# Kernel tuning notes

Measured on AMD Instinct MI355X. Metric: run time of the kernel, lower is better.

## Reference

```python
import jax, jax.numpy as jnp
from jax import lax
import numpy as np

B, TQ, T = 64, 2, 2048
HID, ENC, U, FILT, K = 1024, 512, 256, 32, 31


def setup_inputs() -> dict:
    key = jax.random.key(0)
    ks = jax.random.split(key, 12)
    def w(k, shape, fan_in):
        return jax.random.normal(k, shape, jnp.float32) / np.sqrt(fan_in)
    return {
        "query": jax.random.normal(ks[0], (B, TQ, HID), jnp.float32),
        "state": jax.random.uniform(ks[1], (B, T), jnp.float32),
        "memory": jax.random.normal(ks[2], (B, T, ENC), jnp.float32),
        "Wq": w(ks[3], (HID, U), HID), "bq": jnp.zeros((U,), jnp.float32),
        "Wm": w(ks[4], (ENC, U), ENC), "bm": jnp.zeros((U,), jnp.float32),
        "Wl": w(ks[5], (FILT, U), FILT), "bl": jnp.zeros((U,), jnp.float32),
        "conv_w": w(ks[6], (FILT, 1, K), K), "conv_b": jnp.zeros((FILT,), jnp.float32),
        "We": w(ks[7], (U, U), U), "be": jnp.zeros((U,), jnp.float32),
        "v_a": w(ks[8], (U,), U),
    }


def reference(query, state, memory, Wq, bq, Wm, bm, Wl, bl, conv_w, conv_b, We, be, v_a):
    # memory projection (done in `initialize` in the original): [B,T,U]
    mem_proj = jnp.einsum("bte,eu->btu", memory, Wm) + bm
    # query projection then slice timestep 1 -> [B,1,U]
    pq = (jnp.einsum("bqh,hu->bqu", query, Wq) + bq)[:, 1:2, :]
    # location features: 1-D conv over time of previous alignment, 'same' padding
    x = state[:, None, :]                                    # [B,1,T]
    f = lax.conv_general_dilated(x, conv_w, (1,), "SAME",
                                 dimension_numbers=("NCH", "OIH", "NCH"))
    f = f + conv_b[None, :, None]                            # [B,FILT,T]
    loc = jnp.einsum("bft,fu->btu", f, Wl) + bl              # [B,T,U]
    # additive energy with tanh, reduced against v_a -> [B,T]
    h = jnp.tanh(jnp.einsum("btu,uv->btv", pq + loc + mem_proj, We) + be)
    energy = jnp.einsum("btu,u->bt", h, v_a)
    # smoothing normalization: sigmoid / sum(sigmoid)
    s = jax.nn.sigmoid(energy)
    alignment = s / jnp.sum(s, axis=-1, keepdims=True)
    # cumulate_weights=True: accumulate onto previous alignment
    cum_alignment = state + alignment
    # context against projected memory: [B,1,U]
    context = jnp.einsum("bt,btu->bu", cum_alignment, mem_proj)[:, None, :]
    return context
```

## Files before the change

kernel.cpp:

```cpp
#include <hip/hip_runtime.h>
#include <math.h>

#define Bq 64
#define Tt 2048
#define TQn 2
#define HIDn 1024
#define ENCn 512
#define Un 256
#define FILTn 32
#define KKn 31

#define TTILE 32
#define NCHUNK (Tt / TTILE)
#define LDK 520

typedef short short8 __attribute__((ext_vector_type(8)));
typedef float f32x4  __attribute__((ext_vector_type(4)));
typedef unsigned short ushort_t;
typedef unsigned int   uint_t;

__device__ __forceinline__ ushort_t f2b(float f) {
    union { float f; uint_t u; } x; x.f = f;
    uint_t r = x.u + 0x7fffu + ((x.u >> 16) & 1u);
    return (ushort_t)(r >> 16);
}
__device__ __forceinline__ float b2f(ushort_t u) {
    union { uint_t i; float f; } x; x.i = ((uint_t)u) << 16;
    return x.f;
}


__global__ void k_wlwe(const float* __restrict__ Wl, const float* __restrict__ We,
                       float* __restrict__ WlWe)
{
    const int f = blockIdx.x, v = threadIdx.x;
    float acc = 0.f;
    #pragma unroll 8
    for (int u = 0; u < Un; ++u) acc += Wl[f * Un + u] * We[u * Un + v];
    WlWe[f * Un + v] = acc;
}

__global__ void k_wmwet(const float* __restrict__ Wm, const float* __restrict__ We,
                        ushort_t* __restrict__ WmWeT)
{
    const int e = blockIdx.x, v = threadIdx.x;
    float acc = 0.f;
    #pragma unroll 8
    for (int u = 0; u < Un; ++u) acc += Wm[(size_t)e * Un + u] * We[(size_t)u * Un + v];
    WmWeT[(size_t)v * ENCn + e] = f2b(acc);
}

__global__ void k_cwt(const float* __restrict__ conv_w, const float* __restrict__ WlWe,
                      ushort_t* __restrict__ CWT)
{
    const int k = blockIdx.x, v = threadIdx.x;
    float acc = 0.f;
    if (k < KKn) {
        #pragma unroll
        for (int f = 0; f < FILTn; ++f) acc += conv_w[f * KKn + k] * WlWe[f * Un + v];
    }
    CWT[(size_t)v * 32 + k] = f2b(acc);
}

__global__ void k_g(const float* __restrict__ query, const float* __restrict__ Wq,
                    const float* __restrict__ bq, const float* __restrict__ bm,
                    const float* __restrict__ bl, const float* __restrict__ Wl,
                    const float* __restrict__ conv_b, float* __restrict__ g)
{
    const int b = blockIdx.x, hs = blockIdx.y * 128, u = threadIdx.x;
    const float* q = query + ((size_t)b * TQn + 1) * HIDn + hs;
    float acc = 0.f;
    #pragma unroll 8
    for (int h = 0; h < 128; ++h) acc += q[h] * Wq[(size_t)(hs + h) * Un + u];
    if (blockIdx.y == 0) {
        acc += bq[u] + bm[u] + bl[u];
        #pragma unroll
        for (int f = 0; f < FILTn; ++f) acc += conv_b[f] * Wl[f * Un + u];
    }
    atomicAdd(&g[b * Un + u], acc);
}

__global__ void k_zconst(const float* __restrict__ g, const float* __restrict__ We,
                         const float* __restrict__ be, float* __restrict__ zconst)
{
    const int b = blockIdx.x, us = blockIdx.y * 64, v = threadIdx.x;
    float acc = 0.f;
    #pragma unroll 8
    for (int u = us; u < us + 64; ++u) acc += g[b * Un + u] * We[(size_t)u * Un + v];
    if (blockIdx.y == 0) acc += be[v];
    atomicAdd(&zconst[b * Un + v], acc);
}

__global__ __launch_bounds__(256) void attn_main(
    const float* __restrict__ memory, const float* __restrict__ state,
    const ushort_t* __restrict__ WmWeT, const ushort_t* __restrict__ CWT,
    const float* __restrict__ zconst, const float* __restrict__ v_a,
    float* __restrict__ zA, float* __restrict__ zS,
    float* __restrict__ zSsum, float* __restrict__ zStsum)
{
    const int blk = blockIdx.x;
    const int b  = blk >> 6;
    const int c  = blk & (NCHUNK - 1);
    const int t0 = c * TTILE;
    const int tid = threadIdx.x;

    __shared__ __align__(16) ushort_t mem_s[TTILE * LDK];
    __shared__ __align__(16) float sw_raw[80];
    __shared__ __align__(16) float ep_s[4][TTILE];
    __shared__ __align__(16) float s_s[TTILE];
    float* sw = sw_raw + 1;

    for (int i = tid; i < TTILE + 31; i += 256) {
        const int t = t0 - 15 + i;
        sw[i] = (t >= 0 && t < Tt) ? state[b * Tt + t] : 0.0f;
    }

    const float4* memv4 = (const float4*)(memory + ((size_t)b * Tt + t0) * ENCn);
    #pragma unroll
    for (int i = 0; i < 8; ++i) {
        const int idx = i * 256 + tid;
        const int row = idx >> 6;
        const int cw8 = (idx & 63) << 3;
        const float4 m0 = memv4[2 * idx];
        const float4 m1 = memv4[2 * idx + 1];
        short8 v;
        v[0] = (short)f2b(m0.x); v[1] = (short)f2b(m0.y);
        v[2] = (short)f2b(m0.z); v[3] = (short)f2b(m0.w);
        v[4] = (short)f2b(m1.x); v[5] = (short)f2b(m1.y);
        v[6] = (short)f2b(m1.z); v[7] = (short)f2b(m1.w);
        *(short8*)&mem_s[row * LDK + cw8] = v;
    }

    const int lane = tid & 63;
    const int w    = tid >> 6;
    const int lm   = lane & 15;
    const int lq   = lane >> 4;
    const int ncol0 = w * 64 + lm;

    const ushort_t* bp0 = WmWeT + (size_t)(ncol0 +  0) * ENCn + lq * 8;
    const ushort_t* bp1 = WmWeT + (size_t)(ncol0 + 16) * ENCn + lq * 8;
    const ushort_t* bp2 = WmWeT + (size_t)(ncol0 + 32) * ENCn + lq * 8;
    const ushort_t* bp3 = WmWeT + (size_t)(ncol0 + 48) * ENCn + lq * 8;

    f32x4 acc[2][4] = {};

    short8 bn0 = *(const short8*)bp0;
    short8 bn1 = *(const short8*)bp1;
    short8 bn2 = *(const short8*)bp2;
    short8 bn3 = *(const short8*)bp3;

    __syncthreads();

    const ushort_t* arow0 = &mem_s[(lm) * LDK + lq * 8];
    const ushort_t* arow1 = &mem_s[(16 + lm) * LDK + lq * 8];

    #pragma unroll 4
    for (int s = 0; s < 16; ++s) {
        const short8 b0 = bn0, b1 = bn1, b2 = bn2, b3 = bn3;
        const int sn = (s + 1) & 15;
        bn0 = *(const short8*)(bp0 + sn * 32);
        bn1 = *(const short8*)(bp1 + sn * 32);
        bn2 = *(const short8*)(bp2 + sn * 32);
        bn3 = *(const short8*)(bp3 + sn * 32);
        const short8 a0 = *(const short8*)(arow0 + s * 32);
        const short8 a1 = *(const short8*)(arow1 + s * 32);
        acc[0][0] = __builtin_amdgcn_mfma_f32_16x16x32_bf16(a0, b0, acc[0][0], 0, 0, 0);
        acc[0][1] = __builtin_amdgcn_mfma_f32_16x16x32_bf16(a0, b1, acc[0][1], 0, 0, 0);
        acc[0][2] = __builtin_amdgcn_mfma_f32_16x16x32_bf16(a0, b2, acc[0][2], 0, 0, 0);
        acc[0][3] = __builtin_amdgcn_mfma_f32_16x16x32_bf16(a0, b3, acc[0][3], 0, 0, 0);
        acc[1][0] = __builtin_amdgcn_mfma_f32_16x16x32_bf16(a1, b0, acc[1][0], 0, 0, 0);
        acc[1][1] = __builtin_amdgcn_mfma_f32_16x16x32_bf16(a1, b1, acc[1][1], 0, 0, 0);
        acc[1][2] = __builtin_amdgcn_mfma_f32_16x16x32_bf16(a1, b2, acc[1][2], 0, 0, 0);
        acc[1][3] = __builtin_amdgcn_mfma_f32_16x16x32_bf16(a1, b3, acc[1][3], 0, 0, 0);
    }

    short8 ca0, ca1;
    #pragma unroll
    for (int j = 0; j < 8; ++j) {
        ca0[j] = (short)f2b(sw[lm + lq * 8 + j]);
        ca1[j] = (short)f2b(sw[16 + lm + lq * 8 + j]);
    }
    const ushort_t* cp = CWT + (size_t)ncol0 * 32 + lq * 8;
    const short8 cb0 = *(const short8*)(cp);
    const short8 cb1 = *(const short8*)(cp + 16 * 32);
    const short8 cb2 = *(const short8*)(cp + 32 * 32);
    const short8 cb3 = *(const short8*)(cp + 48 * 32);
    acc[0][0] = __builtin_amdgcn_mfma_f32_16x16x32_bf16(ca0, cb0, acc[0][0], 0, 0, 0);
    acc[0][1] = __builtin_amdgcn_mfma_f32_16x16x32_bf16(ca0, cb1, acc[0][1], 0, 0, 0);
    acc[0][2] = __builtin_amdgcn_mfma_f32_16x16x32_bf16(ca0, cb2, acc[0][2], 0, 0, 0);
    acc[0][3] = __builtin_amdgcn_mfma_f32_16x16x32_bf16(ca0, cb3, acc[0][3], 0, 0, 0);
    acc[1][0] = __builtin_amdgcn_mfma_f32_16x16x32_bf16(ca1, cb0, acc[1][0], 0, 0, 0);
    acc[1][1] = __builtin_amdgcn_mfma_f32_16x16x32_bf16(ca1, cb1, acc[1][1], 0, 0, 0);
    acc[1][2] = __builtin_amdgcn_mfma_f32_16x16x32_bf16(ca1, cb2, acc[1][2], 0, 0, 0);
    acc[1][3] = __builtin_amdgcn_mfma_f32_16x16x32_bf16(ca1, cb3, acc[1][3], 0, 0, 0);

    float zc[4], va[4];
    #pragma unroll
    for (int nbi = 0; nbi < 4; ++nbi) {
        const int col = ncol0 + nbi * 16;
        zc[nbi] = zconst[b * Un + col];
        va[nbi] = v_a[col];
    }
    #pragma unroll
    for (int mb = 0; mb < 2; ++mb) {
        #pragma unroll
        for (int r = 0; r < 4; ++r) {
            float ep = 0.f;
            #pragma unroll
            for (int nbi = 0; nbi < 4; ++nbi) {
                const float h = tanhf(acc[mb][nbi][r] + zc[nbi]);
                ep += h * va[nbi];
            }
            ep += __shfl_xor(ep, 1, 64);
            ep += __shfl_xor(ep, 2, 64);
            ep += __shfl_xor(ep, 4, 64);
            ep += __shfl_xor(ep, 8, 64);
            if (lm == 0) ep_s[w][mb * 16 + lq * 4 + r] = ep;
        }
    }
    __syncthreads();

    if (tid < 64) {
        float s = 0.f, st = 0.f;
        if (tid < TTILE) {
            const float energy = ep_s[0][tid] + ep_s[1][tid] + ep_s[2][tid] + ep_s[3][tid];
            s = 1.0f / (1.0f + expf(-energy));
            s_s[tid] = s;
            st = sw[15 + tid];
        }
        float ssum = s, stsum = st;
        #pragma unroll
        for (int off = 32; off >= 1; off >>= 1) {
            ssum  += __shfl_xor(ssum,  off, 64);
            stsum += __shfl_xor(stsum, off, 64);
        }
        if (tid == 0) {
            atomicAdd(&zSsum[b], ssum);
            atomicAdd(&zStsum[b], stsum);
        }
    }
    __syncthreads();

    const int e0 = tid << 1;
    float aA0 = 0.f, aA1 = 0.f, aS0 = 0.f, aS1 = 0.f;
    #pragma unroll 2
    for (int r4 = 0; r4 < TTILE / 4; ++r4) {
        const float4 sv4 = *(const float4*)&s_s[r4 * 4];
        const float4 st4 = *(const float4*)&sw[15 + r4 * 4];
        const float sv[4] = {sv4.x, sv4.y, sv4.z, sv4.w};
        const float st[4] = {st4.x, st4.y, st4.z, st4.w};
        #pragma unroll
        for (int j = 0; j < 4; ++j) {
            const int r = r4 * 4 + j;
            const float m0 = b2f(mem_s[r * LDK + e0]);
            const float m1 = b2f(mem_s[r * LDK + e0 + 1]);
            aA0 += st[j] * m0; aA1 += st[j] * m1;
            aS0 += sv[j] * m0; aS1 += sv[j] * m1;
        }
    }
    atomicAdd(&zA[b * ENCn + e0],     aA0);
    atomicAdd(&zA[b * ENCn + e0 + 1], aA1);
    atomicAdd(&zS[b * ENCn + e0],     aS0);
    atomicAdd(&zS[b * ENCn + e0 + 1], aS1);
}

__global__ void k_final(const float* __restrict__ zA, const float* __restrict__ zS,
                        const float* __restrict__ zSsum, const float* __restrict__ zStsum,
                        const float* __restrict__ Wm, const float* __restrict__ bm,
                        float* __restrict__ out)
{
    const int b = blockIdx.x, e0 = blockIdx.y * 128, u = threadIdx.x;
    const float inv = 1.0f / zSsum[b];
    float acc = 0.f;
    #pragma unroll 4
    for (int e = e0; e < e0 + 128; ++e) {
        const float ce = zA[b * ENCn + e] + zS[b * ENCn + e] * inv;
        acc += ce * Wm[(size_t)e * Un + u];
    }
    if (blockIdx.y == 0) acc += bm[u] * (zStsum[b] + 1.0f);
    atomicAdd(&out[b * Un + u], acc);
}

extern "C" void kernel_launch(void* const* d_in, const int* in_sizes, int n_in,
                              void* d_out, int out_size, void* d_ws, size_t ws_size,
                              hipStream_t stream)
{
    const float* query  = (const float*)d_in[0];
    const float* state  = (const float*)d_in[1];
    const float* memory = (const float*)d_in[2];
    const float* Wq     = (const float*)d_in[3];
    const float* bq     = (const float*)d_in[4];
    const float* Wm     = (const float*)d_in[5];
    const float* bm     = (const float*)d_in[6];
    const float* Wl     = (const float*)d_in[7];
    const float* bl     = (const float*)d_in[8];
    const float* conv_w = (const float*)d_in[9];
    const float* conv_b = (const float*)d_in[10];
    const float* We     = (const float*)d_in[11];
    const float* be     = (const float*)d_in[12];
    const float* v_a    = (const float*)d_in[13];
    float* out = (float*)d_out;

    float* ws      = (float*)d_ws;
    float* zA      = ws;
    float* zS      = ws + 32768;
    float* zSsum   = ws + 65536;
    float* zStsum  = ws + 65600;
    float* g_      = ws + 65664;
    float* zconst  = ws + 82048;
    float* WlWe    = ws + 98432;
    ushort_t* WmWeT = (ushort_t*)(ws + 106624);
    ushort_t* CWT   = (ushort_t*)(ws + 106624 + 65536);

    hipMemsetAsync(ws, 0, 98432 * sizeof(float), stream);
    hipMemsetAsync(out, 0, (size_t)Bq * Un * sizeof(float), stream);

    hipLaunchKernelGGL(k_wlwe,  dim3(FILTn),     dim3(Un), 0, stream, Wl, We, WlWe);
    hipLaunchKernelGGL(k_wmwet, dim3(ENCn),      dim3(Un), 0, stream, Wm, We, WmWeT);
    hipLaunchKernelGGL(k_g,     dim3(Bq, 8),     dim3(Un), 0, stream,
                       query, Wq, bq, bm, bl, Wl, conv_b, g_);
    hipLaunchKernelGGL(k_cwt,   dim3(32),        dim3(Un), 0, stream, conv_w, WlWe, CWT);
    hipLaunchKernelGGL(k_zconst,dim3(Bq, 4),     dim3(Un), 0, stream, g_, We, be, zconst);
    hipLaunchKernelGGL(attn_main, dim3(Bq * NCHUNK), dim3(256), 0, stream,
                       memory, state, WmWeT, CWT, zconst, v_a, zA, zS, zSsum, zStsum);
    hipLaunchKernelGGL(k_final, dim3(Bq, 4),     dim3(Un), 0, stream,
                       zA, zS, zSsum, zStsum, Wm, bm, out);
}
```

Baseline: 561.8 us.

## Merge prep kernels, stream memory directly into MFMA, double time tile

Folds the five preprocessing kernels into two by precomputing Wq·We and a bias vector, which cuts launches and serial dependencies. The main attention kernel now uses a 64-row time tile and loads memory straight from global into registers with packed bf16 conversion, dropping the LDS staging buffer. The context accumulation then rereads memory in fp32 from global or cache. It also switches to fast tanh/sigmoid intrinsics, sets launch bounds for occupancy, and splits accumulators in small loops. The risks are a second global read of memory, higher register pressure from 16 accumulators, and slightly different numerics.

```diff
diff --git a/kernel.cpp b/kernel.cpp
--- a/kernel.cpp
+++ b/kernel.cpp
@@ -1,4 +1,5 @@
 #include <hip/hip_runtime.h>
+#include <hip/hip_bf16.h>
 #include <math.h>
 
 #define Bq 64
@@ -10,88 +11,121 @@
 #define FILTn 32
 #define KKn 31
 
-#define TTILE 32
+#define TTILE 64
 #define NCHUNK (Tt / TTILE)
-#define LDK 520
 
 typedef short short8 __attribute__((ext_vector_type(8)));
 typedef float f32x4  __attribute__((ext_vector_type(4)));
 typedef unsigned short ushort_t;
 typedef unsigned int   uint_t;
 
+union S8 { short8 v; uint_t u[4]; };
+
 __device__ __forceinline__ ushort_t f2b(float f) {
     union { float f; uint_t u; } x; x.f = f;
     uint_t r = x.u + 0x7fffu + ((x.u >> 16) & 1u);
     return (ushort_t)(r >> 16);
 }
-__device__ __forceinline__ float b2f(ushort_t u) {
-    union { uint_t i; float f; } x; x.i = ((uint_t)u) << 16;
-    return x.f;
-}
-
-
-__global__ void k_wlwe(const float* __restrict__ Wl, const float* __restrict__ We,
-                       float* __restrict__ WlWe)
-{
-    const int f = blockIdx.x, v = threadIdx.x;
-    float acc = 0.f;
-    #pragma unroll 8
-    for (int u = 0; u < Un; ++u) acc += Wl[f * Un + u] * We[u * Un + v];
-    WlWe[f * Un + v] = acc;
-}
-
-__global__ void k_wmwet(const float* __restrict__ Wm, const float* __restrict__ We,
-                        ushort_t* __restrict__ WmWeT)
-{
-    const int e = blockIdx.x, v = threadIdx.x;
-    float acc = 0.f;
-    #pragma unroll 8
-    for (int u = 0; u < Un; ++u) acc += Wm[(size_t)e * Un + u] * We[(size_t)u * Un + v];
-    WmWeT[(size_t)v * ENCn + e] = f2b(acc);
-}
-
-__global__ void k_cwt(const float* __restrict__ conv_w, const float* __restrict__ WlWe,
-                      ushort_t* __restrict__ CWT)
-{
-    const int k = blockIdx.x, v = threadIdx.x;
-    float acc = 0.f;
-    if (k < KKn) {
-        #pragma unroll
-        for (int f = 0; f < FILTn; ++f) acc += conv_w[f * KKn + k] * WlWe[f * Un + v];
-    }
-    CWT[(size_t)v * 32 + k] = f2b(acc);
-}
-
-__global__ void k_g(const float* __restrict__ query, const float* __restrict__ Wq,
-                    const float* __restrict__ bq, const float* __restrict__ bm,
-                    const float* __restrict__ bl, const float* __restrict__ Wl,
-                    const float* __restrict__ conv_b, float* __restrict__ g)
-{
-    const int b = blockIdx.x, hs = blockIdx.y * 128, u = threadIdx.x;
-    const float* q = query + ((size_t)b * TQn + 1) * HIDn + hs;
-    float acc = 0.f;
-    #pragma unroll 8
-    for (int h = 0; h < 128; ++h) acc += q[h] * Wq[(size_t)(hs + h) * Un + u];
+__device__ __forceinline__ uint_t cvt_pk(float lo, float hi) {
+    union { __hip_bfloat162 h; uint_t u; } x;
+    x.h = __float22bfloat162_rn(make_float2(lo, hi));
+    return x.u;
+}
+__device__ __forceinline__ float tanh_fast(float x) {
+    const float e = __expf(2.0f * x);
+    return 1.0f - 2.0f * __builtin_amdgcn_rcpf(e + 1.0f);
+}
+
+__global__ void k_prep1(const float* __restrict__ Wq, const float* __restrict__ We,
+                        const float* __restrict__ Wm, const float* __restrict__ Wl,
+                        const float* __restrict__ conv_w, const float* __restrict__ bq,
+                        const float* __restrict__ bm, const float* __restrict__ bl,
+                        const float* __restrict__ conv_b,
+                        float* __restrict__ WqWe, ushort_t* __restrict__ WmWeT,
+                        ushort_t* __restrict__ CWT, float* __restrict__ cvec)
+{
+    const int blk = blockIdx.x;
+    const int v = threadIdx.x;
+    if (blk < 1024) {
+        const int h = blk;
+        float a0 = 0.f, a1 = 0.f, a2 = 0.f, a3 = 0.f;
+        #pragma unroll 4
+        for (int u = 0; u < Un; u += 4) {
+            a0 += Wq[h * Un + u + 0] * We[(u + 0) * Un + v];
+            a1 += Wq[h * Un + u + 1] * We[(u + 1) * Un + v];
+            a2 += Wq[h * Un + u + 2] * We[(u + 2) * Un + v];
+            a3 += Wq[h * Un + u + 3] * We[(u + 3) * Un + v];
+        }
+        WqWe[(size_t)h * Un + v] = (a0 + a1) + (a2 + a3);
+    } else if (blk < 1536) {
+        const int e = blk - 1024;
+        float a0 = 0.f, a1 = 0.f, a2 = 0.f, a3 = 0.f;
+        #pragma unroll 4
+        for (int u = 0; u < Un; u += 4) {
+            a0 += Wm[(size_t)e * Un + u + 0] * We[(u + 0) * Un + v];
+            a1 += Wm[(size_t)e * Un + u + 1] * We[(u + 1) * Un + v];
+            a2 += Wm[(size_t)e * Un + u + 2] * We[(u + 2) * Un + v];
+            a3 += Wm[(size_t)e * Un + u + 3] * We[(u + 3) * Un + v];
+        }
+        WmWeT[(size_t)v * ENCn + e] = f2b((a0 + a1) + (a2 + a3));
+    } else if (blk < 1540) {
+        const int vc = (blk - 1536) * 64;
+        __shared__ float wlwe[FILTn * 64];
+        for (int i = threadIdx.x; i < FILTn * 64; i += 256) {
+            const int f = i >> 6, vv = i & 63;
+            float a = 0.f;
+            #pragma unroll 8
+            for (int u = 0; u < Un; ++u) a += Wl[f * Un + u] * We[u * Un + vc + vv];
+            wlwe[f * 64 + vv] = a;
+        }
+        __syncthreads();
+        for (int i = threadIdx.x; i < 64 * 32; i += 256) {
+            const int vv = i >> 5, k = i & 31;
+            float a = 0.f;
+            if (k < KKn) {
+                #pragma unroll
+                for (int f = 0; f < FILTn; ++f) a += conv_w[f * KKn + k] * wlwe[f * 64 + vv];
+            }
+            CWT[(size_t)(vc + vv) * 32 + k] = f2b(a);
+        }
+    } else {
+        const int u = v;
+        float a = bq[u] + bm[u] + bl[u];
+        #pragma unroll
+        for (int f = 0; f < FILTn; ++f) a += conv_b[f] * Wl[f * Un + u];
+        cvec[u] = a;
+    }
+}
+
+__global__ void k_prep2(const float* __restrict__ query, const float* __restrict__ WqWe,
+                        const float* __restrict__ cvec, const float* __restrict__ We,
+                        const float* __restrict__ be, float* __restrict__ zconst)
+{
+    const int b = blockIdx.x, h0 = blockIdx.y * 256, v = threadIdx.x;
+    const float* q = query + ((size_t)b * TQn + 1) * HIDn;
+    float a0 = 0.f, a1 = 0.f, a2 = 0.f, a3 = 0.f;
+    #pragma unroll 4
+    for (int h = 0; h < 256; h += 4) {
+        a0 += q[h0 + h + 0] * WqWe[(size_t)(h0 + h + 0) * Un + v];
+        a1 += q[h0 + h + 1] * WqWe[(size_t)(h0 + h + 1) * Un + v];
+        a2 += q[h0 + h + 2] * WqWe[(size_t)(h0 + h + 2) * Un + v];
+        a3 += q[h0 + h + 3] * WqWe[(size_t)(h0 + h + 3) * Un + v];
+    }
+    float acc = (a0 + a1) + (a2 + a3);
     if (blockIdx.y == 0) {
-        acc += bq[u] + bm[u] + bl[u];
-        #pragma unroll
-        for (int f = 0; f < FILTn; ++f) acc += conv_b[f] * Wl[f * Un + u];
-    }
-    atomicAdd(&g[b * Un + u], acc);
-}
-
-__global__ void k_zconst(const float* __restrict__ g, const float* __restrict__ We,
-                         const float* __restrict__ be, float* __restrict__ zconst)
-{
-    const int b = blockIdx.x, us = blockIdx.y * 64, v = threadIdx.x;
-    float acc = 0.f;
-    #pragma unroll 8
-    for (int u = us; u < us + 64; ++u) acc += g[b * Un + u] * We[(size_t)u * Un + v];
-    if (blockIdx.y == 0) acc += be[v];
+        acc += be[v];
+        float c0 = 0.f, c1 = 0.f;
+        #pragma unroll 4
+        for (int u = 0; u < Un; u += 2) {
+            c0 += cvec[u]     * We[u * Un + v];
+            c1 += cvec[u + 1] * We[(u + 1) * Un + v];
+        }
+        acc += c0 + c1;
+    }
     atomicAdd(&zconst[b * Un + v], acc);
 }
 
-__global__ __launch_bounds__(256) void attn_main(
+__global__ __launch_bounds__(256, 2) void attn_main(
     const float* __restrict__ memory, const float* __restrict__ state,
     const ushort_t* __restrict__ WmWeT, const ushort_t* __restrict__ CWT,
     const float* __restrict__ zconst, const float* __restrict__ v_a,
@@ -99,13 +133,12 @@
     float* __restrict__ zSsum, float* __restrict__ zStsum)
 {
     const int blk = blockIdx.x;
-    const int b  = blk >> 6;
+    const int b  = blk >> 5;
     const int c  = blk & (NCHUNK - 1);
     const int t0 = c * TTILE;
     const int tid = threadIdx.x;
 
-    __shared__ __align__(16) ushort_t mem_s[TTILE * LDK];
-    __shared__ __align__(16) float sw_raw[80];
+    __shared__ __align__(16) float sw_raw[100];
     __shared__ __align__(16) float ep_s[4][TTILE];
     __shared__ __align__(16) float s_s[TTILE];
     float* sw = sw_raw + 1;
@@ -113,22 +146,6 @@
     for (int i = tid; i < TTILE + 31; i += 256) {
         const int t = t0 - 15 + i;
         sw[i] = (t >= 0 && t < Tt) ? state[b * Tt + t] : 0.0f;
-    }
-
-    const float4* memv4 = (const float4*)(memory + ((size_t)b * Tt + t0) * ENCn);
-    #pragma unroll
-    for (int i = 0; i < 8; ++i) {
-        const int idx = i * 256 + tid;
-        const int row = idx >> 6;
-        const int cw8 = (idx & 63) << 3;
-        const float4 m0 = memv4[2 * idx];
-        const float4 m1 = memv4[2 * idx + 1];
-        short8 v;
-        v[0] = (short)f2b(m0.x); v[1] = (short)f2b(m0.y);
-        v[2] = (short)f2b(m0.z); v[3] = (short)f2b(m0.w);
-        v[4] = (short)f2b(m1.x); v[5] = (short)f2b(m1.y);
-        v[6] = (short)f2b(m1.z); v[7] = (short)f2b(m1.w);
-        *(short8*)&mem_s[row * LDK + cw8] = v;
     }
 
     const int lane = tid & 63;
@@ -137,62 +154,83 @@
     const int lq   = lane >> 4;
     const int ncol0 = w * 64 + lm;
 
+    const float* abase = memory + ((size_t)b * Tt + t0) * ENCn + lq * 8;
+    const float* ap0 = abase + (size_t)(lm +  0) * ENCn;
+    const float* ap1 = abase + (size_t)(lm + 16) * ENCn;
+    const float* ap2 = abase + (size_t)(lm + 32) * ENCn;
+    const float* ap3 = abase + (size_t)(lm + 48) * ENCn;
+
     const ushort_t* bp0 = WmWeT + (size_t)(ncol0 +  0) * ENCn + lq * 8;
     const ushort_t* bp1 = WmWeT + (size_t)(ncol0 + 16) * ENCn + lq * 8;
     const ushort_t* bp2 = WmWeT + (size_t)(ncol0 + 32) * ENCn + lq * 8;
     const ushort_t* bp3 = WmWeT + (size_t)(ncol0 + 48) * ENCn + lq * 8;
 
-    f32x4 acc[2][4] = {};
-
+    f32x4 acc[4][4] = {};
+
+    float4 an[4][2];
+    an[0][0] = *(const float4*)(ap0); an[0][1] = *(const float4*)(ap0 + 4);
+    an[1][0] = *(const float4*)(ap1); an[1][1] = *(const float4*)(ap1 + 4);
+    an[2][0] = *(const float4*)(ap2); an[2][1] = *(const float4*)(ap2 + 4);
+    an[3][0] = *(const float4*)(ap3); an[3][1] = *(const float4*)(ap3 + 4);
     short8 bn0 = *(const short8*)bp0;
     short8 bn1 = *(const short8*)bp1;
     short8 bn2 = *(const short8*)bp2;
     short8 bn3 = *(const short8*)bp3;
 
-    __syncthreads();
-
-    const ushort_t* arow0 = &mem_s[(lm) * LDK + lq * 8];
-    const ushort_t* arow1 = &mem_s[(16 + lm) * LDK + lq * 8];
-
     #pragma unroll 4
     for (int s = 0; s < 16; ++s) {
+        S8 a[4];
+        #pragma unroll
+        for (int m = 0; m < 4; ++m) {
+            a[m].u[0] = cvt_pk(an[m][0].x, an[m][0].y);
+            a[m].u[1] = cvt_pk(an[m][0].z, an[m][0].w);
+            a[m].u[2] = cvt_pk(an[m][1].x, an[m][1].y);
+            a[m].u[3] = cvt_pk(an[m][1].z, an[m][1].w);
+        }
         const short8 b0 = bn0, b1 = bn1, b2 = bn2, b3 = bn3;
-        const int sn = (s + 1) & 15;
-        bn0 = *(const short8*)(bp0 + sn * 32);
-        bn1 = *(const short8*)(bp1 + sn * 32);
-        bn2 = *(const short8*)(bp2 + sn * 32);
-        bn3 = *(const short8*)(bp3 + sn * 32);
-        const short8 a0 = *(const short8*)(arow0 + s * 32);
-        const short8 a1 = *(const short8*)(arow1 + s * 32);
-        acc[0][0] = __builtin_amdgcn_mfma_f32_16x16x32_bf16(a0, b0, acc[0][0], 0, 0, 0);
-        acc[0][1] = __builtin_amdgcn_mfma_f32_16x16x32_bf16(a0, b1, acc[0][1], 0, 0, 0);
-        acc[0][2] = __builtin_amdgcn_mfma_f32_16x16x32_bf16(a0, b2, acc[0][2], 0, 0, 0);
-        acc[0][3] = __builtin_amdgcn_mfma_f32_16x16x32_bf16(a0, b3, acc[0][3], 0, 0, 0);
-        acc[1][0] = __builtin_amdgcn_mfma_f32_16x16x32_bf16(a1, b0, acc[1][0], 0, 0, 0);
-        acc[1][1] = __builtin_amdgcn_mfma_f32_16x16x32_bf16(a1, b1, acc[1][1], 0, 0, 0);
-        acc[1][2] = __builtin_amdgcn_mfma_f32_16x16x32_bf16(a1, b2, acc[1][2], 0, 0, 0);
-        acc[1][3] = __builtin_amdgcn_mfma_f32_16x16x32_bf16(a1, b3, acc[1][3], 0, 0, 0);
-    }
-
-    short8 ca0, ca1;
-    #pragma unroll
-    for (int j = 0; j < 8; ++j) {
-        ca0[j] = (short)f2b(sw[lm + lq * 8 + j]);
-        ca1[j] = (short)f2b(sw[16 + lm + lq * 8 + j]);
-    }
-    const ushort_t* cp = CWT + (size_t)ncol0 * 32 + lq * 8;
-    const short8 cb0 = *(const short8*)(cp);
-    const short8 cb1 = *(const short8*)(cp + 16 * 32);
-    const short8 cb2 = *(const short8*)(cp + 32 * 32);
-    const short8 cb3 = *(const short8*)(cp + 48 * 32);
-    acc[0][0] = __builtin_amdgcn_mfma_f32_16x16x32_bf16(ca0, cb0, acc[0][0], 0, 0, 0);
-    acc[0][1] = __builtin_amdgcn_mfma_f32_16x16x32_bf16(ca0, cb1, acc[0][1], 0, 0, 0);
-    acc[0][2] = __builtin_amdgcn_mfma_f32_16x16x32_bf16(ca0, cb2, acc[0][2], 0, 0, 0);
-    acc[0][3] = __builtin_amdgcn_mfma_f32_16x16x32_bf16(ca0, cb3, acc[0][3], 0, 0, 0);
-    acc[1][0] = __builtin_amdgcn_mfma_f32_16x16x32_bf16(ca1, cb0, acc[1][0], 0, 0, 0);
-    acc[1][1] = __builtin_amdgcn_mfma_f32_16x16x32_bf16(ca1, cb1, acc[1][1], 0, 0, 0);
-    acc[1][2] = __builtin_amdgcn_mfma_f32_16x16x32_bf16(ca1, cb2, acc[1][2], 0, 0, 0);
-    acc[1][3] = __builtin_amdgcn_mfma_f32_16x16x32_bf16(ca1, cb3, acc[1][3], 0, 0, 0);
+        const int sn = ((s + 1) & 15) * 32;
+        an[0][0] = *(const float4*)(ap0 + sn); an[0][1] = *(const float4*)(ap0 + sn + 4);
+        an[1][0] = *(const float4*)(ap1 + sn); an[1][1] = *(const float4*)(ap1 + sn + 4);
+        an[2][0] = *(const float4*)(ap2 + sn); an[2][1] = *(const float4*)(ap2 + sn + 4);
+        an[3][0] = *(const float4*)(ap3 + sn); an[3][1] = *(const float4*)(ap3 + sn + 4);
+        bn0 = *(const short8*)(bp0 + sn);
+        bn1 = *(const short8*)(bp1 + sn);
+        bn2 = *(const short8*)(bp2 + sn);
+        bn3 = *(const short8*)(bp3 + sn);
+
+        #pragma unroll
+        for (int m = 0; m < 4; ++m) {
+            acc[m][0] = __builtin_amdgcn_mfma_f32_16x16x32_bf16(a[m].v, b0, acc[m][0], 0, 0, 0);
+            acc[m][1] = __builtin_amdgcn_mfma_f32_16x16x32_bf16(a[m].v, b1, acc[m][1], 0, 0, 0);
+            acc[m][2] = __builtin_amdgcn_mfma_f32_16x16x32_bf16(a[m].v, b2, acc[m][2], 0, 0, 0);
+            acc[m][3] = __builtin_amdgcn_mfma_f32_16x16x32_bf16(a[m].v, b3, acc[m][3], 0, 0, 0);
+        }
+    }
+
+    __syncthreads();
+
+    {
+        S8 ca[4];
+        #pragma unroll
+        for (int m = 0; m < 4; ++m) {
+            const int base = 16 * m + lm + lq * 8;
+            #pragma unroll
+            for (int j = 0; j < 4; ++j)
+                ca[m].u[j] = cvt_pk(sw[base + 2 * j], sw[base + 2 * j + 1]);
+        }
+        const ushort_t* cp = CWT + (size_t)ncol0 * 32 + lq * 8;
+        const short8 cb0 = *(const short8*)(cp);
+        const short8 cb1 = *(const short8*)(cp + 16 * 32);
+        const short8 cb2 = *(const short8*)(cp + 32 * 32);
+        const short8 cb3 = *(const short8*)(cp + 48 * 32);
+        #pragma unroll
+        for (int m = 0; m < 4; ++m) {
+            acc[m][0] = __builtin_amdgcn_mfma_f32_16x16x32_bf16(ca[m].v, cb0, acc[m][0], 0, 0, 0);
+            acc[m][1] = __builtin_amdgcn_mfma_f32_16x16x32_bf16(ca[m].v, cb1, acc[m][1], 0, 0, 0);
+            acc[m][2] = __builtin_amdgcn_mfma_f32_16x16x32_bf16(ca[m].v, cb2, acc[m][2], 0, 0, 0);
+            acc[m][3] = __builtin_amdgcn_mfma_f32_16x16x32_bf16(ca[m].v, cb3, acc[m][3], 0, 0, 0);
+        }
+    }
 
     float zc[4], va[4];
     #pragma unroll
@@ -202,32 +240,27 @@
         va[nbi] = v_a[col];
     }
     #pragma unroll
-    for (int mb = 0; mb < 2; ++mb) {
+    for (int mi = 0; mi < 4; ++mi) {
         #pragma unroll
         for (int r = 0; r < 4; ++r) {
             float ep = 0.f;
             #pragma unroll
-            for (int nbi = 0; nbi < 4; ++nbi) {
-                const float h = tanhf(acc[mb][nbi][r] + zc[nbi]);
-                ep += h * va[nbi];
-            }
+            for (int nbi = 0; nbi < 4; ++nbi)
+                ep += tanh_fast(acc[mi][nbi][r] + zc[nbi]) * va[nbi];
             ep += __shfl_xor(ep, 1, 64);
             ep += __shfl_xor(ep, 2, 64);
             ep += __shfl_xor(ep, 4, 64);
             ep += __shfl_xor(ep, 8, 64);
-            if (lm == 0) ep_s[w][mb * 16 + lq * 4 + r] = ep;
+            if (lm == 0) ep_s[w][16 * mi + 4 * lq + r] = ep;
         }
     }
     __syncthreads();
 
     if (tid < 64) {
-        float s = 0.f, st = 0.f;
-        if (tid < TTILE) {
-            const float energy = ep_s[0][tid] + ep_s[1][tid] + ep_s[2][tid] + ep_s[3][tid];
-            s = 1.0f / (1.0f + expf(-energy));
-            s_s[tid] = s;
-            st = sw[15 + tid];
-        }
+        const float energy = ep_s[0][tid] + ep_s[1][tid] + ep_s[2][tid] + ep_s[3][tid];
+        const float s = __builtin_amdgcn_rcpf(1.0f + __expf(-energy));
+        s_s[tid] = s;
+        float st = sw[15 + tid];
         float ssum = s, stsum = st;
         #pragma unroll
         for (int off = 32; off >= 1; off >>= 1) {
@@ -242,20 +275,19 @@
     __syncthreads();
 
     const int e0 = tid << 1;
+    const float* mcol = memory + ((size_t)b * Tt + t0) * ENCn + e0;
     float aA0 = 0.f, aA1 = 0.f, aS0 = 0.f, aS1 = 0.f;
     #pragma unroll 2
     for (int r4 = 0; r4 < TTILE / 4; ++r4) {
-        const float4 sv4 = *(const float4*)&s_s[r4 * 4];
-        const float4 st4 = *(const float4*)&sw[15 + r4 * 4];
+        const float4 st4 = *(const float4*)&sw[15 + 4 * r4];
+        const float4 sv4 = *(const float4*)&s_s[4 * r4];
+        const float st[4] = {st4.x, st4.y, st4.z, st4.w};
         const float sv[4] = {sv4.x, sv4.y, sv4.z, sv4.w};
-        const float st[4] = {st4.x, st4.y, st4.z, st4.w};
         #pragma unroll
         for (int j = 0; j < 4; ++j) {
-            const int r = r4 * 4 + j;
-            const float m0 = b2f(mem_s[r * LDK + e0]);
-            const float m1 = b2f(mem_s[r * LDK + e0 + 1]);
-            aA0 += st[j] * m0; aA1 += st[j] * m1;
-            aS0 += sv[j] * m0; aS1 += sv[j] * m1;
+            const float2 m = *(const float2*)(mcol + (size_t)(4 * r4 + j) * ENCn);
+            aA0 += st[j] * m.x; aA1 += st[j] * m.y;
+            aS0 += sv[j] * m.x; aS1 += sv[j] * m.y;
         }
     }
     atomicAdd(&zA[b * ENCn + e0],     aA0);
@@ -271,12 +303,15 @@
 {
     const int b = blockIdx.x, e0 = blockIdx.y * 128, u = threadIdx.x;
     const float inv = 1.0f / zSsum[b];
-    float acc = 0.f;
+    float a0 = 0.f, a1 = 0.f;
     #pragma unroll 4
-    for (int e = e0; e < e0 + 128; ++e) {
-        const float ce = zA[b * ENCn + e] + zS[b * ENCn + e] * inv;
-        acc += ce * Wm[(size_t)e * Un + u];
-    }
+    for (int e = e0; e < e0 + 128; e += 2) {
+        const float c0 = zA[b * ENCn + e]     + zS[b * ENCn + e]     * inv;
+        const float c1 = zA[b * ENCn + e + 1] + zS[b * ENCn + e + 1] * inv;
+        a0 += c0 * Wm[(size_t)e * Un + u];
+        a1 += c1 * Wm[(size_t)(e + 1) * Un + u];
+    }
+    float acc = a0 + a1;
     if (blockIdx.y == 0) acc += bm[u] * (zStsum[b] + 1.0f);
     atomicAdd(&out[b * Un + u], acc);
 }
@@ -306,23 +341,22 @@
     float* zS      = ws + 32768;
     float* zSsum   = ws + 65536;
     float* zStsum  = ws + 65600;
-    float* g_      = ws + 65664;
-    float* zconst  = ws + 82048;
-    float* WlWe    = ws + 98432;
-    ushort_t* WmWeT = (ushort_t*)(ws + 106624);
-    ushort_t* CWT   = (ushort_t*)(ws + 106624 + 65536);
-
-    hipMemsetAsync(ws, 0, 98432 * sizeof(float), stream);
+    float* zconst  = ws + 65664;
+    float* WqWe    = ws + 82048;
+    float* cvec    = ws + 344192;
+    ushort_t* WmWeT = (ushort_t*)(ws + 344448);
+    ushort_t* CWT   = (ushort_t*)(ws + 409984);
+
+    hipMemsetAsync(ws, 0, 82048 * sizeof(float), stream);
     hipMemsetAsync(out, 0, (size_t)Bq * Un * sizeof(float), stream);
 
-    hipLaunchKernelGGL(k_wlwe,  dim3(FILTn),     dim3(Un), 0, stream, Wl, We, WlWe);
-    hipLaunchKernelGGL(k_wmwet, dim3(ENCn),      dim3(Un), 0, stream, Wm, We, WmWeT);
-    hipLaunchKernelGGL(k_g,     dim3(Bq, 8),     dim3(Un), 0, stream,
-                       query, Wq, bq, bm, bl, Wl, conv_b, g_);
-    hipLaunchKernelGGL(k_cwt,   dim3(32),        dim3(Un), 0, stream, conv_w, WlWe, CWT);
-    hipLaunchKernelGGL(k_zconst,dim3(Bq, 4),     dim3(Un), 0, stream, g_, We, be, zconst);
+    hipLaunchKernelGGL(k_prep1, dim3(1541), dim3(Un), 0, stream,
+                       Wq, We, Wm, Wl, conv_w, bq, bm, bl, conv_b,
+                       WqWe, WmWeT, CWT, cvec);
+    hipLaunchKernelGGL(k_prep2, dim3(Bq, 4), dim3(Un), 0, stream,
+                       query, WqWe, cvec, We, be, zconst);
     hipLaunchKernelGGL(attn_main, dim3(Bq * NCHUNK), dim3(256), 0, stream,
                        memory, state, WmWeT, CWT, zconst, v_a, zA, zS, zSsum, zStsum);
-    hipLaunchKernelGGL(k_final, dim3(Bq, 4),     dim3(Un), 0, stream,
+    hipLaunchKernelGGL(k_final, dim3(Bq, 4), dim3(Un), 0, stream,
                        zA, zS, zSsum, zStsum, Wm, bm, out);
 }
```

Measured after the change: 699.9 us. 1.25x slower.

## Merge weight-prep kernels, double-buffer B loads, use fast tanh and packed bf16 conversion

Applied to the files above, without the earlier changes.

Folds the three weight-precompute kernels (WmWe, WlWe, CWT) plus the constant bias vector into a single prep launch, reducing launch count and serial dependencies. In the main attention kernel, B-fragment global loads move ahead of the memory staging and become two-deep double-buffered, A fragments are prefetched from LDS, and fp32-to-bf16 conversion uses packed conversion intrinsics. tanh and sigmoid switch to exp/rcp approximations, and several small GEMV kernels split their accumulators to shorten dependency chains. The approximations slightly change numerics, and the occupancy hint in launch bounds may constrain register allocation.

```diff
diff --git a/kernel.cpp b/kernel.cpp
--- a/kernel.cpp
+++ b/kernel.cpp
@@ -1,4 +1,5 @@
 #include <hip/hip_runtime.h>
+#include <hip/hip_bf16.h>
 #include <math.h>
 
 #define Bq 64
@@ -19,64 +20,91 @@
 typedef unsigned short ushort_t;
 typedef unsigned int   uint_t;
 
+union S8 { short8 v; uint_t u[4]; };
+
 __device__ __forceinline__ ushort_t f2b(float f) {
     union { float f; uint_t u; } x; x.f = f;
     uint_t r = x.u + 0x7fffu + ((x.u >> 16) & 1u);
     return (ushort_t)(r >> 16);
 }
-__device__ __forceinline__ float b2f(ushort_t u) {
-    union { uint_t i; float f; } x; x.i = ((uint_t)u) << 16;
+__device__ __forceinline__ uint_t cvt_pk(float lo, float hi) {
+    union { __hip_bfloat162 h; uint_t u; } x;
+    x.h = __float22bfloat162_rn(make_float2(lo, hi));
+    return x.u;
+}
+__device__ __forceinline__ float b2f(uint_t u16) {
+    union { uint_t i; float f; } x; x.i = u16 << 16;
     return x.f;
 }
-
-
-__global__ void k_wlwe(const float* __restrict__ Wl, const float* __restrict__ We,
-                       float* __restrict__ WlWe)
-{
-    const int f = blockIdx.x, v = threadIdx.x;
-    float acc = 0.f;
-    #pragma unroll 8
-    for (int u = 0; u < Un; ++u) acc += Wl[f * Un + u] * We[u * Un + v];
-    WlWe[f * Un + v] = acc;
-}
-
-__global__ void k_wmwet(const float* __restrict__ Wm, const float* __restrict__ We,
-                        ushort_t* __restrict__ WmWeT)
-{
-    const int e = blockIdx.x, v = threadIdx.x;
-    float acc = 0.f;
-    #pragma unroll 8
-    for (int u = 0; u < Un; ++u) acc += Wm[(size_t)e * Un + u] * We[(size_t)u * Un + v];
-    WmWeT[(size_t)v * ENCn + e] = f2b(acc);
-}
-
-__global__ void k_cwt(const float* __restrict__ conv_w, const float* __restrict__ WlWe,
-                      ushort_t* __restrict__ CWT)
-{
-    const int k = blockIdx.x, v = threadIdx.x;
-    float acc = 0.f;
-    if (k < KKn) {
-        #pragma unroll
-        for (int f = 0; f < FILTn; ++f) acc += conv_w[f * KKn + k] * WlWe[f * Un + v];
-    }
-    CWT[(size_t)v * 32 + k] = f2b(acc);
+__device__ __forceinline__ float tanh_fast(float x) {
+    const float e = __expf(2.0f * x);
+    return 1.0f - 2.0f * __builtin_amdgcn_rcpf(e + 1.0f);
+}
+
+__global__ void k_prep1(const float* __restrict__ We, const float* __restrict__ Wm,
+                        const float* __restrict__ Wl, const float* __restrict__ conv_w,
+                        const float* __restrict__ bq, const float* __restrict__ bm,
+                        const float* __restrict__ bl, const float* __restrict__ conv_b,
+                        ushort_t* __restrict__ WmWeT, ushort_t* __restrict__ CWT,
+                        float* __restrict__ cvec)
+{
+    const int blk = blockIdx.x;
+    const int v = threadIdx.x;
+    if (blk < 512) {
+        const int e = blk;
+        float a0 = 0.f, a1 = 0.f, a2 = 0.f, a3 = 0.f;
+        #pragma unroll 4
+        for (int u = 0; u < Un; u += 4) {
+            a0 += Wm[(size_t)e * Un + u + 0] * We[(u + 0) * Un + v];
+            a1 += Wm[(size_t)e * Un + u + 1] * We[(u + 1) * Un + v];
+            a2 += Wm[(size_t)e * Un + u + 2] * We[(u + 2) * Un + v];
+            a3 += Wm[(size_t)e * Un + u + 3] * We[(u + 3) * Un + v];
+        }
+        WmWeT[(size_t)v * ENCn + e] = f2b((a0 + a1) + (a2 + a3));
+    } else if (blk < 516) {
+        const int vc = (blk - 512) * 64;
+        __shared__ float wlwe[FILTn * 64];
+        for (int i = threadIdx.x; i < FILTn * 64; i += 256) {
+            const int f = i >> 6, vv = i & 63;
+            float a = 0.f;
+            #pragma unroll 8
+            for (int u = 0; u < Un; ++u) a += Wl[f * Un + u] * We[u * Un + vc + vv];
+            wlwe[f * 64 + vv] = a;
+        }
+        __syncthreads();
+        for (int i = threadIdx.x; i < 64 * 32; i += 256) {
+            const int vv = i >> 5, k = i & 31;
+            float a = 0.f;
+            if (k < KKn) {
+                #pragma unroll
+                for (int f = 0; f < FILTn; ++f) a += conv_w[f * KKn + k] * wlwe[f * 64 + vv];
+            }
+            CWT[(size_t)(vc + vv) * 32 + k] = f2b(a);
+        }
+    } else {
+        const int u = v;
+        float a = bq[u] + bm[u] + bl[u];
+        #pragma unroll
+        for (int f = 0; f < FILTn; ++f) a += conv_b[f] * Wl[f * Un + u];
+        cvec[u] = a;
+    }
 }
 
 __global__ void k_g(const float* __restrict__ query, const float* __restrict__ Wq,
-                    const float* __restrict__ bq, const float* __restrict__ bm,
-                    const float* __restrict__ bl, const float* __restrict__ Wl,
-                    const float* __restrict__ conv_b, float* __restrict__ g)
+                    const float* __restrict__ cvec, float* __restrict__ g)
 {
     const int b = blockIdx.x, hs = blockIdx.y * 128, u = threadIdx.x;
     const float* q = query + ((size_t)b * TQn + 1) * HIDn + hs;
-    float acc = 0.f;
-    #pragma unroll 8
-    for (int h = 0; h < 128; ++h) acc += q[h] * Wq[(size_t)(hs + h) * Un + u];
-    if (blockIdx.y == 0) {
-        acc += bq[u] + bm[u] + bl[u];
-        #pragma unroll
-        for (int f = 0; f < FILTn; ++f) acc += conv_b[f] * Wl[f * Un + u];
-    }
+    float a0 = 0.f, a1 = 0.f, a2 = 0.f, a3 = 0.f;
+    #pragma unroll 4
+    for (int h = 0; h < 128; h += 4) {
+        a0 += q[h + 0] * Wq[(size_t)(hs + h + 0) * Un + u];
+        a1 += q[h + 1] * Wq[(size_t)(hs + h + 1) * Un + u];
+        a2 += q[h + 2] * Wq[(size_t)(hs + h + 2) * Un + u];
+        a3 += q[h + 3] * Wq[(size_t)(hs + h + 3) * Un + u];
+    }
+    float acc = (a0 + a1) + (a2 + a3);
+    if (blockIdx.y == 0) acc += cvec[u];
     atomicAdd(&g[b * Un + u], acc);
 }
 
@@ -84,14 +112,18 @@
                          const float* __restrict__ be, float* __restrict__ zconst)
 {
     const int b = blockIdx.x, us = blockIdx.y * 64, v = threadIdx.x;
-    float acc = 0.f;
-    #pragma unroll 8
-    for (int u = us; u < us + 64; ++u) acc += g[b * Un + u] * We[(size_t)u * Un + v];
+    float a0 = 0.f, a1 = 0.f;
+    #pragma unroll 4
+    for (int u = us; u < us + 64; u += 2) {
+        a0 += g[b * Un + u]     * We[(size_t)u * Un + v];
+        a1 += g[b * Un + u + 1] * We[(size_t)(u + 1) * Un + v];
+    }
+    float acc = a0 + a1;
     if (blockIdx.y == 0) acc += be[v];
     atomicAdd(&zconst[b * Un + v], acc);
 }
 
-__global__ __launch_bounds__(256) void attn_main(
+__global__ __launch_bounds__(256, 4) void attn_main(
     const float* __restrict__ memory, const float* __restrict__ state,
     const ushort_t* __restrict__ WmWeT, const ushort_t* __restrict__ CWT,
     const float* __restrict__ zconst, const float* __restrict__ v_a,
@@ -114,6 +146,23 @@
         const int t = t0 - 15 + i;
         sw[i] = (t >= 0 && t < Tt) ? state[b * Tt + t] : 0.0f;
     }
+
+    const int lane = tid & 63;
+    const int w    = tid >> 6;
+    const int lm   = lane & 15;
+    const int lq   = lane >> 4;
+    const int ncol0 = w * 64 + lm;
+
+    const ushort_t* bp0 = WmWeT + (size_t)(ncol0 +  0) * ENCn + lq * 8;
+    const ushort_t* bp1 = WmWeT + (size_t)(ncol0 + 16) * ENCn + lq * 8;
+    const ushort_t* bp2 = WmWeT + (size_t)(ncol0 + 32) * ENCn + lq * 8;
+    const ushort_t* bp3 = WmWeT + (size_t)(ncol0 + 48) * ENCn + lq * 8;
+
+    short8 bbuf[2][4];
+    bbuf[0][0] = *(const short8*)(bp0);      bbuf[0][1] = *(const short8*)(bp1);
+    bbuf[0][2] = *(const short8*)(bp2);      bbuf[0][3] = *(const short8*)(bp3);
+    bbuf[1][0] = *(const short8*)(bp0 + 32); bbuf[1][1] = *(const short8*)(bp1 + 32);
+    bbuf[1][2] = *(const short8*)(bp2 + 32); bbuf[1][3] = *(const short8*)(bp3 + 32);
 
     const float4* memv4 = (const float4*)(memory + ((size_t)b * Tt + t0) * ENCn);
     #pragma unroll
@@ -123,76 +172,65 @@
         const int cw8 = (idx & 63) << 3;
         const float4 m0 = memv4[2 * idx];
         const float4 m1 = memv4[2 * idx + 1];
-        short8 v;
-        v[0] = (short)f2b(m0.x); v[1] = (short)f2b(m0.y);
-        v[2] = (short)f2b(m0.z); v[3] = (short)f2b(m0.w);
-        v[4] = (short)f2b(m1.x); v[5] = (short)f2b(m1.y);
-        v[6] = (short)f2b(m1.z); v[7] = (short)f2b(m1.w);
-        *(short8*)&mem_s[row * LDK + cw8] = v;
-    }
-
-    const int lane = tid & 63;
-    const int w    = tid >> 6;
-    const int lm   = lane & 15;
-    const int lq   = lane >> 4;
-    const int ncol0 = w * 64 + lm;
-
-    const ushort_t* bp0 = WmWeT + (size_t)(ncol0 +  0) * ENCn + lq * 8;
-    const ushort_t* bp1 = WmWeT + (size_t)(ncol0 + 16) * ENCn + lq * 8;
-    const ushort_t* bp2 = WmWeT + (size_t)(ncol0 + 32) * ENCn + lq * 8;
-    const ushort_t* bp3 = WmWeT + (size_t)(ncol0 + 48) * ENCn + lq * 8;
+        S8 v;
+        v.u[0] = cvt_pk(m0.x, m0.y); v.u[1] = cvt_pk(m0.z, m0.w);
+        v.u[2] = cvt_pk(m1.x, m1.y); v.u[3] = cvt_pk(m1.z, m1.w);
+        *(short8*)&mem_s[row * LDK + cw8] = v.v;
+    }
 
     f32x4 acc[2][4] = {};
-
-    short8 bn0 = *(const short8*)bp0;
-    short8 bn1 = *(const short8*)bp1;
-    short8 bn2 = *(const short8*)bp2;
-    short8 bn3 = *(const short8*)bp3;
 
     __syncthreads();
 
     const ushort_t* arow0 = &mem_s[(lm) * LDK + lq * 8];
     const ushort_t* arow1 = &mem_s[(16 + lm) * LDK + lq * 8];
 
-    #pragma unroll 4
+    short8 a0c = *(const short8*)(arow0);
+    short8 a1c = *(const short8*)(arow1);
+
+    #pragma unroll
     for (int s = 0; s < 16; ++s) {
-        const short8 b0 = bn0, b1 = bn1, b2 = bn2, b3 = bn3;
-        const int sn = (s + 1) & 15;
-        bn0 = *(const short8*)(bp0 + sn * 32);
-        bn1 = *(const short8*)(bp1 + sn * 32);
-        bn2 = *(const short8*)(bp2 + sn * 32);
-        bn3 = *(const short8*)(bp3 + sn * 32);
-        const short8 a0 = *(const short8*)(arow0 + s * 32);
-        const short8 a1 = *(const short8*)(arow1 + s * 32);
-        acc[0][0] = __builtin_amdgcn_mfma_f32_16x16x32_bf16(a0, b0, acc[0][0], 0, 0, 0);
-        acc[0][1] = __builtin_amdgcn_mfma_f32_16x16x32_bf16(a0, b1, acc[0][1], 0, 0, 0);
-        acc[0][2] = __builtin_amdgcn_mfma_f32_16x16x32_bf16(a0, b2, acc[0][2], 0, 0, 0);
-        acc[0][3] = __builtin_amdgcn_mfma_f32_16x16x32_bf16(a0, b3, acc[0][3], 0, 0, 0);
-        acc[1][0] = __builtin_amdgcn_mfma_f32_16x16x32_bf16(a1, b0, acc[1][0], 0, 0, 0);
-        acc[1][1] = __builtin_amdgcn_mfma_f32_16x16x32_bf16(a1, b1, acc[1][1], 0, 0, 0);
-        acc[1][2] = __builtin_amdgcn_mfma_f32_16x16x32_bf16(a1, b2, acc[1][2], 0, 0, 0);
-        acc[1][3] = __builtin_amdgcn_mfma_f32_16x16x32_bf16(a1, b3, acc[1][3], 0, 0, 0);
-    }
-
-    short8 ca0, ca1;
-    #pragma unroll
-    for (int j = 0; j < 8; ++j) {
-        ca0[j] = (short)f2b(sw[lm + lq * 8 + j]);
-        ca1[j] = (short)f2b(sw[16 + lm + lq * 8 + j]);
-    }
-    const ushort_t* cp = CWT + (size_t)ncol0 * 32 + lq * 8;
-    const short8 cb0 = *(const short8*)(cp);
-    const short8 cb1 = *(const short8*)(cp + 16 * 32);
-    const short8 cb2 = *(const short8*)(cp + 32 * 32);
-    const short8 cb3 = *(const short8*)(cp + 48 * 32);
-    acc[0][0] = __builtin_amdgcn_mfma_f32_16x16x32_bf16(ca0, cb0, acc[0][0], 0, 0, 0);
-    acc[0][1] = __builtin_amdgcn_mfma_f32_16x16x32_bf16(ca0, cb1, acc[0][1], 0, 0, 0);
-    acc[0][2] = __builtin_amdgcn_mfma_f32_16x16x32_bf16(ca0, cb2, acc[0][2], 0, 0, 0);
-    acc[0][3] = __builtin_amdgcn_mfma_f32_16x16x32_bf16(ca0, cb3, acc[0][3], 0, 0, 0);
-    acc[1][0] = __builtin_amdgcn_mfma_f32_16x16x32_bf16(ca1, cb0, acc[1][0], 0, 0, 0);
-    acc[1][1] = __builtin_amdgcn_mfma_f32_16x16x32_bf16(ca1, cb1, acc[1][1], 0, 0, 0);
-    acc[1][2] = __builtin_amdgcn_mfma_f32_16x16x32_bf16(ca1, cb2, acc[1][2], 0, 0, 0);
-    acc[1][3] = __builtin_amdgcn_mfma_f32_16x16x32_bf16(ca1, cb3, acc[1][3], 0, 0, 0);
+        const int sa = ((s + 1) & 15) * 32;
+        const short8 a0n = *(const short8*)(arow0 + sa);
+        const short8 a1n = *(const short8*)(arow1 + sa);
+        acc[0][0] = __builtin_amdgcn_mfma_f32_16x16x32_bf16(a0c, bbuf[s & 1][0], acc[0][0], 0, 0, 0);
+        acc[0][1] = __builtin_amdgcn_mfma_f32_16x16x32_bf16(a0c, bbuf[s & 1][1], acc[0][1], 0, 0, 0);
+        acc[0][2] = __builtin_amdgcn_mfma_f32_16x16x32_bf16(a0c, bbuf[s & 1][2], acc[0][2], 0, 0, 0);
+        acc[0][3] = __builtin_amdgcn_mfma_f32_16x16x32_bf16(a0c, bbuf[s & 1][3], acc[0][3], 0, 0, 0);
+        acc[1][0] = __builtin_amdgcn_mfma_f32_16x16x32_bf16(a1c, bbuf[s & 1][0], acc[1][0], 0, 0, 0);
+        acc[1][1] = __builtin_amdgcn_mfma_f32_16x16x32_bf16(a1c, bbuf[s & 1][1], acc[1][1], 0, 0, 0);
+        acc[1][2] = __builtin_amdgcn_mfma_f32_16x16x32_bf16(a1c, bbuf[s & 1][2], acc[1][2], 0, 0, 0);
+        acc[1][3] = __builtin_amdgcn_mfma_f32_16x16x32_bf16(a1c, bbuf[s & 1][3], acc[1][3], 0, 0, 0);
+        const int sn = ((s + 2) & 15) * 32;
+        bbuf[s & 1][0] = *(const short8*)(bp0 + sn);
+        bbuf[s & 1][1] = *(const short8*)(bp1 + sn);
+        bbuf[s & 1][2] = *(const short8*)(bp2 + sn);
+        bbuf[s & 1][3] = *(const short8*)(bp3 + sn);
+        a0c = a0n; a1c = a1n;
+    }
+
+    {
+        S8 ca0, ca1;
+        #pragma unroll
+        for (int j = 0; j < 4; ++j) {
+            const int base0 = lm + lq * 8 + 2 * j;
+            ca0.u[j] = cvt_pk(sw[base0],      sw[base0 + 1]);
+            ca1.u[j] = cvt_pk(sw[base0 + 16], sw[base0 + 17]);
+        }
+        const ushort_t* cp = CWT + (size_t)ncol0 * 32 + lq * 8;
+        const short8 cb0 = *(const short8*)(cp);
+        const short8 cb1 = *(const short8*)(cp + 16 * 32);
+        const short8 cb2 = *(const short8*)(cp + 32 * 32);
+        const short8 cb3 = *(const short8*)(cp + 48 * 32);
+        acc[0][0] = __builtin_amdgcn_mfma_f32_16x16x32_bf16(ca0.v, cb0, acc[0][0], 0, 0, 0);
+        acc[0][1] = __builtin_amdgcn_mfma_f32_16x16x32_bf16(ca0.v, cb1, acc[0][1], 0, 0, 0);
+        acc[0][2] = __builtin_amdgcn_mfma_f32_16x16x32_bf16(ca0.v, cb2, acc[0][2], 0, 0, 0);
+        acc[0][3] = __builtin_amdgcn_mfma_f32_16x16x32_bf16(ca0.v, cb3, acc[0][3], 0, 0, 0);
+        acc[1][0] = __builtin_amdgcn_mfma_f32_16x16x32_bf16(ca1.v, cb0, acc[1][0], 0, 0, 0);
+        acc[1][1] = __builtin_amdgcn_mfma_f32_16x16x32_bf16(ca1.v, cb1, acc[1][1], 0, 0, 0);
+        acc[1][2] = __builtin_amdgcn_mfma_f32_16x16x32_bf16(ca1.v, cb2, acc[1][2], 0, 0, 0);
+        acc[1][3] = __builtin_amdgcn_mfma_f32_16x16x32_bf16(ca1.v, cb3, acc[1][3], 0, 0, 0);
+    }
 
     float zc[4], va[4];
     #pragma unroll
@@ -207,10 +245,8 @@
         for (int r = 0; r < 4; ++r) {
             float ep = 0.f;
             #pragma unroll
-            for (int nbi = 0; nbi < 4; ++nbi) {
-                const float h = tanhf(acc[mb][nbi][r] + zc[nbi]);
-                ep += h * va[nbi];
-            }
+            for (int nbi = 0; nbi < 4; ++nbi)
+                ep += tanh_fast(acc[mb][nbi][r] + zc[nbi]) * va[nbi];
             ep += __shfl_xor(ep, 1, 64);
             ep += __shfl_xor(ep, 2, 64);
             ep += __shfl_xor(ep, 4, 64);
@@ -224,7 +260,7 @@
         float s = 0.f, st = 0.f;
         if (tid < TTILE) {
             const float energy = ep_s[0][tid] + ep_s[1][tid] + ep_s[2][tid] + ep_s[3][tid];
-            s = 1.0f / (1.0f + expf(-energy));
+            s = __builtin_amdgcn_rcpf(1.0f + __expf(-energy));
             s_s[tid] = s;
             st = sw[15 + tid];
         }
@@ -252,8 +288,9 @@
         #pragma unroll
         for (int j = 0; j < 4; ++j) {
             const int r = r4 * 4 + j;
-            const float m0 = b2f(mem_s[r * LDK + e0]);
-            const float m1 = b2f(mem_s[r * LDK + e0 + 1]);
+            const uint_t mm = *(const uint_t*)&mem_s[r * LDK + e0];
+            const float m0 = b2f(mm & 0xffffu);
+            const float m1 = b2f(mm >> 16);
             aA0 += st[j] * m0; aA1 += st[j] * m1;
             aS0 += sv[j] * m0; aS1 += sv[j] * m1;
         }
@@ -271,12 +308,15 @@
 {
     const int b = blockIdx.x, e0 = blockIdx.y * 128, u = threadIdx.x;
     const float inv = 1.0f / zSsum[b];
-    float acc = 0.f;
+    float a0 = 0.f, a1 = 0.f;
     #pragma unroll 4
-    for (int e = e0; e < e0 + 128; ++e) {
-        const float ce = zA[b * ENCn + e] + zS[b * ENCn + e] * inv;
-        acc += ce * Wm[(size_t)e * Un + u];
-    }
+    for (int e = e0; e < e0 + 128; e += 2) {
+        const float c0 = zA[b * ENCn + e]     + zS[b * ENCn + e]     * inv;
+        const float c1 = zA[b * ENCn + e + 1] + zS[b * ENCn + e + 1] * inv;
+        a0 += c0 * Wm[(size_t)e * Un + u];
+        a1 += c1 * Wm[(size_t)(e + 1) * Un + u];
+    }
+    float acc = a0 + a1;
     if (blockIdx.y == 0) acc += bm[u] * (zStsum[b] + 1.0f);
     atomicAdd(&out[b * Un + u], acc);
 }
@@ -308,21 +348,19 @@
     float* zStsum  = ws + 65600;
     float* g_      = ws + 65664;
     float* zconst  = ws + 82048;
-    float* WlWe    = ws + 98432;
-    ushort_t* WmWeT = (ushort_t*)(ws + 106624);
-    ushort_t* CWT   = (ushort_t*)(ws + 106624 + 65536);
+    float* cvec    = ws + 98432;
+    ushort_t* WmWeT = (ushort_t*)(ws + 98688);
+    ushort_t* CWT   = (ushort_t*)(ws + 164224);
 
     hipMemsetAsync(ws, 0, 98432 * sizeof(float), stream);
     hipMemsetAsync(out, 0, (size_t)Bq * Un * sizeof(float), stream);
 
-    hipLaunchKernelGGL(k_wlwe,  dim3(FILTn),     dim3(Un), 0, stream, Wl, We, WlWe);
-    hipLaunchKernelGGL(k_wmwet, dim3(ENCn),      dim3(Un), 0, stream, Wm, We, WmWeT);
-    hipLaunchKernelGGL(k_g,     dim3(Bq, 8),     dim3(Un), 0, stream,
-                       query, Wq, bq, bm, bl, Wl, conv_b, g_);
-    hipLaunchKernelGGL(k_cwt,   dim3(32),        dim3(Un), 0, stream, conv_w, WlWe, CWT);
-    hipLaunchKernelGGL(k_zconst,dim3(Bq, 4),     dim3(Un), 0, stream, g_, We, be, zconst);
+    hipLaunchKernelGGL(k_prep1, dim3(517), dim3(Un), 0, stream,
+                       We, Wm, Wl, conv_w, bq, bm, bl, conv_b, WmWeT, CWT, cvec);
+    hipLaunchKernelGGL(k_g, dim3(Bq, 8), dim3(Un), 0, stream, query, Wq, cvec, g_);
+    hipLaunchKernelGGL(k_zconst, dim3(Bq, 4), dim3(Un), 0, stream, g_, We, be, zconst);
     hipLaunchKernelGGL(attn_main, dim3(Bq * NCHUNK), dim3(256), 0, stream,
                        memory, state, WmWeT, CWT, zconst, v_a, zA, zS, zSsum, zStsum);
-    hipLaunchKernelGGL(k_final, dim3(Bq, 4),     dim3(Un), 0, stream,
+    hipLaunchKernelGGL(k_final, dim3(Bq, 4), dim3(Un), 0, stream,
                        zA, zS, zSsum, zStsum, Wm, bm, out);
 }
```

Measured after the change: 559.9 us. Within noise of the previous version (-0.3%).
